# Optimization experiments

Hardware: AMD Instinct MI355X
Metric: run time of the kernel (lower is better)

Reference implementation:

```python
import jax, jax.numpy as jnp
import numpy as np

N_NODES = 50000
N_INC = 300000
IN_DIM = 256
OUT_DIM = 256
NEG_SLOPE = 0.2
BN_EPS = 1e-5


def setup_inputs() -> dict:
    key = jax.random.key(0)
    ks = jax.random.split(key, 8)
    x = jax.random.normal(ks[0], (N_NODES, IN_DIM), dtype=jnp.float32)
    node_idx = jax.random.randint(ks[1], (N_INC,), 0, N_NODES)
    edge_idx = jax.random.randint(ks[2], (N_INC,), 0, 20000)
    W = jax.random.normal(ks[3], (IN_DIM, OUT_DIM), dtype=jnp.float32) / np.sqrt(IN_DIM)
    att = jax.random.normal(ks[4], (2 * OUT_DIM,), dtype=jnp.float32) * 0.1
    bias = jnp.zeros((OUT_DIM,), dtype=jnp.float32)
    gamma = jnp.ones((OUT_DIM,), dtype=jnp.float32)
    beta = jnp.zeros((OUT_DIM,), dtype=jnp.float32)
    return {
        'x': x, 'node_idx': node_idx, 'edge_idx': edge_idx,
        'num_hyperedges': 20000,
        'W': W, 'att': att, 'bias': bias, 'gamma': gamma, 'beta': beta,
    }


def reference(x, node_idx, edge_idx, num_hyperedges, W, att, bias, gamma, beta):
    N = x.shape[0]
    M = num_hyperedges
    xw = x @ W                                  # [N, D]

    # attention over incidences (old-PyG: edge feature := node feature at edge id)
    x_i = xw[node_idx]                          # [E, D]
    x_j = xw[edge_idx]                          # [E, D]
    alpha = jnp.sum(jnp.concatenate([x_i, x_j], axis=-1) * att, axis=-1)  # [E]
    alpha = jax.nn.leaky_relu(alpha, NEG_SLOPE)
    # segment softmax grouped by node index
    amax = jax.ops.segment_max(alpha, node_idx, num_segments=N)
    amax = jnp.where(jnp.isfinite(amax), amax, 0.0)
    e = jnp.exp(alpha - amax[node_idx])
    esum = jax.ops.segment_sum(e, node_idx, num_segments=N)
    alpha = e / (esum[node_idx] + 1e-16)        # [E]

    ones = jnp.ones_like(alpha)
    Dn = jax.ops.segment_sum(ones, node_idx, num_segments=N)   # node degree
    Dinv = jnp.where(Dn > 0, 1.0 / Dn, 0.0)
    Be = jax.ops.segment_sum(ones, edge_idx, num_segments=M)   # edge degree
    Binv = jnp.where(Be > 0, 1.0 / Be, 0.0)

    # stage 1: node -> hyperedge, norm = B at target edge
    msg1 = (Binv[edge_idx] * alpha)[:, None] * x_i              # [E, D]
    edge_feat = jax.ops.segment_sum(msg1, edge_idx, num_segments=M)  # [M, D]

    # stage 2: hyperedge -> node, norm = D at target node
    msg2 = (Dinv[node_idx] * alpha)[:, None] * edge_feat[edge_idx]   # [E, D]
    out = jax.ops.segment_sum(msg2, node_idx, num_segments=N) + bias  # [N, D]

    # BatchNorm1d (training: batch stats, biased variance) + ELU
    mu = jnp.mean(out, axis=0)
    var = jnp.mean((out - mu) ** 2, axis=0)
    out = gamma * (out - mu) * jax.lax.rsqrt(var + BN_EPS) + beta
    return jax.nn.elu(out)
```

## Files before the change

kernel.cpp:

```cpp
#include <hip/hip_runtime.h>

#define N_NODES 50000
#define N_INC   300000
#define DIM     256
#define M_EDGES 20000
#define NEG_SLOPE 0.2f
#define BN_EPS  1e-5f
#define EBLK 20
#define NBLK 49

typedef __attribute__((ext_vector_type(8))) short short8;
typedef __attribute__((ext_vector_type(4))) float f32x4;

__device__ __forceinline__ unsigned bf16rn(float f) {
    unsigned u = __float_as_uint(f);
    return (u + 0x7FFFu + ((u >> 16) & 1u)) >> 16;
}
__device__ __forceinline__ float4 unp4(uint2 p) {
    return make_float4(__uint_as_float(p.x << 16),
                       __uint_as_float(p.x & 0xFFFF0000u),
                       __uint_as_float(p.y << 16),
                       __uint_as_float(p.y & 0xFFFF0000u));
}

__global__ void wt_kernel(const float* __restrict__ W, ushort* __restrict__ WT)
{
    int i = blockIdx.x * 256 + threadIdx.x;
    int k = i >> 8, n = i & 255;
    WT[n * 256 + k] = (ushort)bf16rn(W[i]);
}

#define GBM 256
__global__ __launch_bounds__(512) void gemm_persist(
    const float* __restrict__ A, const ushort* __restrict__ WT,
    const float* __restrict__ att,
    ushort* __restrict__ xwb, float* __restrict__ s1, float* __restrict__ s2)
{
    __shared__ __align__(16) char Bs[131072];
    int tid = threadIdx.x;
    int lane = tid & 63, w = tid >> 6;

    #pragma unroll
    for (int i = 0; i < 16; ++i) {
        int flat = tid + 512 * i;
        int n = flat >> 5, kc = flat & 31;
        uint4 v = *(const uint4*)(WT + n * 256 + kc * 8);
        int off = n * 512 + ((kc * 16) ^ ((n & 7) << 4));
        *(uint4*)(Bs + off) = v;
    }
    __syncthreads();

    int row0 = blockIdx.x * GBM + w * 32;

    short8 afrag[2][8];
    #pragma unroll
    for (int j = 0; j < 8; ++j) {
        #pragma unroll
        for (int s = 0; s < 2; ++s) {
            int row = row0 + s * 16 + (lane & 15);
            float4 u0 = make_float4(0.f, 0.f, 0.f, 0.f), u1 = u0;
            if (row < N_NODES) {
                const float* p = A + (size_t)row * DIM + j * 32 + (lane >> 4) * 8;
                u0 = *(const float4*)p;
                u1 = *(const float4*)(p + 4);
            }
            uint4 q;
            q.x = bf16rn(u0.x) | (bf16rn(u0.y) << 16);
            q.y = bf16rn(u0.z) | (bf16rn(u0.w) << 16);
            q.z = bf16rn(u1.x) | (bf16rn(u1.y) << 16);
            q.w = bf16rn(u1.z) | (bf16rn(u1.w) << 16);
            afrag[s][j] = *(short8*)&q;
        }
    }

    float p1a[2][4] = {}, p2a[2][4] = {};
    #pragma unroll
    for (int ch = 0; ch < 2; ++ch) {
        f32x4 acc[2][8] = {};
        #pragma unroll
        for (int j = 0; j < 8; ++j) {
            int kb = j * 64 + (lane >> 4) * 16;
            #pragma unroll
            for (int c = 0; c < 8; ++c) {
                int col = ch * 128 + c * 16 + (lane & 15);
                short8 b = *(const short8*)(Bs + col * 512 + (kb ^ ((col & 7) << 4)));
                acc[0][c] = __builtin_amdgcn_mfma_f32_16x16x32_bf16(afrag[0][j], b, acc[0][c], 0, 0, 0);
                acc[1][c] = __builtin_amdgcn_mfma_f32_16x16x32_bf16(afrag[1][j], b, acc[1][c], 0, 0, 0);
            }
        }
        #pragma unroll
        for (int c = 0; c < 8; ++c) {
            int col = ch * 128 + c * 16 + (lane & 15);
            float a1 = att[col], a2 = att[DIM + col];
            #pragma unroll
            for (int s = 0; s < 2; ++s)
                #pragma unroll
                for (int r = 0; r < 4; ++r) {
                    int row = row0 + s * 16 + (lane >> 4) * 4 + r;
                    float v = acc[s][c][r];
                    if (row < N_NODES)
                        xwb[(size_t)row * DIM + col] = (ushort)bf16rn(v);
                    p1a[s][r] += v * a1;
                    p2a[s][r] += v * a2;
                }
        }
    }
    #pragma unroll
    for (int s = 0; s < 2; ++s)
        #pragma unroll
        for (int r = 0; r < 4; ++r) {
            float p1 = p1a[s][r], p2 = p2a[s][r];
            #pragma unroll
            for (int msk = 1; msk < 16; msk <<= 1) {
                p1 += __shfl_xor(p1, msk);
                p2 += __shfl_xor(p2, msk);
            }
            int row = row0 + s * 16 + (lane >> 4) * 4 + r;
            if ((lane & 15) == 0 && row < N_NODES) {
                s1[row] = p1;
                s2[row] = p2;
            }
        }
}

__global__ void rank_kernel(
    const int* __restrict__ node_idx, const int* __restrict__ edge_idx,
    const float* __restrict__ s1, const float* __restrict__ s2,
    float* __restrict__ ealpha, unsigned* __restrict__ rank_pk,
    int* __restrict__ cnt_n, int* __restrict__ cnt_e)
{
    int e = blockIdx.x * blockDim.x + threadIdx.x;
    if (e >= N_INC) return;
    int n = node_idx[e], h = edge_idx[e];
    float a = s1[n] + s2[h];
    a = a > 0.f ? a : NEG_SLOPE * a;
    ealpha[e] = __expf(a);
    unsigned rn = (unsigned)atomicAdd(cnt_n + n, 1);
    unsigned re = (unsigned)atomicAdd(cnt_e + h, 1);
    rank_pk[e] = (re << 16) | rn;
}

__global__ __launch_bounds__(1024) void scan_partial(
    const int* __restrict__ cnt_e, int* __restrict__ start_e, int* __restrict__ totals_e,
    const int* __restrict__ cnt_n, int* __restrict__ start_n, int* __restrict__ totals_n)
{
    int b = blockIdx.x;
    const int* cnt; int* start; int* totals; int n; int cb;
    if (b < EBLK) { cnt = cnt_e; start = start_e; totals = totals_e; n = M_EDGES; cb = b; }
    else          { cnt = cnt_n; start = start_n; totals = totals_n; n = N_NODES; cb = b - EBLK; }
    int tid = threadIdx.x, lane = tid & 63, wid = tid >> 6;
    int i = cb * 1024 + tid;
    int v = (i < n) ? cnt[i] : 0;
    #pragma unroll
    for (int off = 1; off < 64; off <<= 1) {
        int t = __shfl_up(v, off);
        if (lane >= off) v += t;
    }
    __shared__ int wsum[16];
    if (lane == 63) wsum[wid] = v;
    __syncthreads();
    if (wid == 0 && lane < 16) {
        int s = wsum[lane];
        #pragma unroll
        for (int off = 1; off < 16; off <<= 1) {
            int t = __shfl_up(s, off);
            if (lane >= off) s += t;
        }
        wsum[lane] = s;
    }
    __syncthreads();
    if (wid > 0) v += wsum[wid - 1];
    if (i < n) start[i + 1] = v;
    if (tid == 1023) totals[cb] = v;
}

__global__ void scan_totals(
    const int* __restrict__ totals_e, int* __restrict__ boff_e,
    const int* __restrict__ totals_n, int* __restrict__ boff_n,
    int* __restrict__ start_e, int* __restrict__ start_n)
{
    int lane = threadIdx.x;
    int ve0 = (lane < EBLK) ? totals_e[lane] : 0;
    int ve = ve0;
    #pragma unroll
    for (int off = 1; off < 64; off <<= 1) {
        int t = __shfl_up(ve, off);
        if (lane >= off) ve += t;
    }
    if (lane < EBLK) boff_e[lane] = ve - ve0;
    int vn0 = (lane < NBLK) ? totals_n[lane] : 0;
    int vn = vn0;
    #pragma unroll
    for (int off = 1; off < 64; off <<= 1) {
        int t = __shfl_up(vn, off);
        if (lane >= off) vn += t;
    }
    if (lane < NBLK) boff_n[lane] = vn - vn0;
    if (lane == 0) { start_e[0] = 0; start_n[0] = 0; }
}

__global__ void scan_add(
    int* __restrict__ start_e, const int* __restrict__ boff_e,
    int* __restrict__ start_n, const int* __restrict__ boff_n)
{
    int id = blockIdx.x * 256 + threadIdx.x;
    if (id < M_EDGES) start_e[id + 1] += boff_e[id >> 10];
    else if (id < M_EDGES + N_NODES) {
        int j = id - M_EDGES;
        start_n[j + 1] += boff_n[j >> 10];
    }
}

__global__ void place_kernel(
    const int* __restrict__ node_idx, const int* __restrict__ edge_idx,
    const unsigned* __restrict__ rank_pk,
    const int* __restrict__ start_e, const int* __restrict__ start_n,
    int* __restrict__ list_e, int* __restrict__ list_n)
{
    int e = blockIdx.x * blockDim.x + threadIdx.x;
    if (e >= N_INC) return;
    unsigned pk = rank_pk[e];
    list_e[start_e[edge_idx[e]] + (pk >> 16)] = e;
    list_n[start_n[node_idx[e]] + (pk & 0xFFFFu)] = e;
}

__global__ void rnorm_kernel(
    const float* __restrict__ ealpha, const int* __restrict__ start_n,
    const int* __restrict__ list_n, float* __restrict__ rnorm)
{
    int n = blockIdx.x * blockDim.x + threadIdx.x;
    if (n >= N_NODES) return;
    int j0 = start_n[n], j1 = start_n[n + 1];
    float s = 0.f;
    for (int j = j0; j < j1; ++j) s += ealpha[list_n[j]];
    rnorm[n] = 1.f / (s + 1e-16f);
}

__global__ __launch_bounds__(256) void stage1_kernel(
    const ushort* __restrict__ xwb, const int* __restrict__ node_idx,
    const float* __restrict__ ealpha, const float* __restrict__ rnorm,
    const int* __restrict__ start_e, const int* __restrict__ list_e,
    ushort* __restrict__ edge_feat)
{
    int h = blockIdx.x * 4 + (threadIdx.x >> 6);
    if (h >= M_EDGES) return;
    int lane = threadIdx.x & 63;
    int j0 = start_e[h], j1 = start_e[h + 1];
    float4 acc = make_float4(0.f, 0.f, 0.f, 0.f);
    float4 ac2 = make_float4(0.f, 0.f, 0.f, 0.f);
    for (int base = j0; base < j1; base += 64) {
        int cnt = min(64, j1 - base);
        float wv = 0.f; int nv = 0;
        if (lane < cnt) {
            int e = list_e[base + lane];
            int n_ = node_idx[e];
            wv = ealpha[e] * rnorm[n_];
            nv = n_;
        }
        int jj = 0;
        for (; jj + 4 <= cnt; jj += 4) {
            float wg0 = __shfl(wv, jj);     int n0 = __shfl(nv, jj);
            float wg1 = __shfl(wv, jj + 1); int n1 = __shfl(nv, jj + 1);
            float wg2 = __shfl(wv, jj + 2); int n2 = __shfl(nv, jj + 2);
            float wg3 = __shfl(wv, jj + 3); int n3 = __shfl(nv, jj + 3);
            uint2 p0 = *(const uint2*)(xwb + (size_t)n0 * DIM + lane * 4);
            uint2 p1 = *(const uint2*)(xwb + (size_t)n1 * DIM + lane * 4);
            uint2 p2 = *(const uint2*)(xwb + (size_t)n2 * DIM + lane * 4);
            uint2 p3 = *(const uint2*)(xwb + (size_t)n3 * DIM + lane * 4);
            float4 v0 = unp4(p0), v1 = unp4(p1), v2 = unp4(p2), v3 = unp4(p3);
            acc.x += wg0 * v0.x + wg1 * v1.x;  ac2.x += wg2 * v2.x + wg3 * v3.x;
            acc.y += wg0 * v0.y + wg1 * v1.y;  ac2.y += wg2 * v2.y + wg3 * v3.y;
            acc.z += wg0 * v0.z + wg1 * v1.z;  ac2.z += wg2 * v2.z + wg3 * v3.z;
            acc.w += wg0 * v0.w + wg1 * v1.w;  ac2.w += wg2 * v2.w + wg3 * v3.w;
        }
        for (; jj < cnt; ++jj) {
            float wg = __shfl(wv, jj); int n0 = __shfl(nv, jj);
            float4 v = unp4(*(const uint2*)(xwb + (size_t)n0 * DIM + lane * 4));
            acc.x += wg * v.x; acc.y += wg * v.y;
            acc.z += wg * v.z; acc.w += wg * v.w;
        }
    }
    acc.x += ac2.x; acc.y += ac2.y; acc.z += ac2.z; acc.w += ac2.w;
    float binv = (j1 > j0) ? 1.f / (float)(j1 - j0) : 0.f;
    uint2 p;
    p.x = bf16rn(acc.x * binv) | (bf16rn(acc.y * binv) << 16);
    p.y = bf16rn(acc.z * binv) | (bf16rn(acc.w * binv) << 16);
    *(uint2*)(edge_feat + (size_t)h * DIM + lane * 4) = p;
}

__global__ __launch_bounds__(256) void stage2_kernel(
    const ushort* __restrict__ edge_feat, const int* __restrict__ edge_idx,
    const float* __restrict__ ealpha, const float* __restrict__ rnorm,
    const int* __restrict__ start_n, const int* __restrict__ list_n,
    const float* __restrict__ bias, float* __restrict__ out)
{
    int n = blockIdx.x * 4 + (threadIdx.x >> 6);
    if (n >= N_NODES) return;
    int lane = threadIdx.x & 63;
    int j0 = start_n[n], j1 = start_n[n + 1];
    float4 acc = make_float4(0.f, 0.f, 0.f, 0.f);
    float4 ac2 = make_float4(0.f, 0.f, 0.f, 0.f);
    for (int base = j0; base < j1; base += 64) {
        int cnt = min(64, j1 - base);
        float wv = 0.f; int hv = 0;
        if (lane < cnt) { int e = list_n[base + lane]; wv = ealpha[e]; hv = edge_idx[e]; }
        int jj = 0;
        for (; jj + 4 <= cnt; jj += 4) {
            float wg0 = __shfl(wv, jj);     int h0 = __shfl(hv, jj);
            float wg1 = __shfl(wv, jj + 1); int h1 = __shfl(hv, jj + 1);
            float wg2 = __shfl(wv, jj + 2); int h2 = __shfl(hv, jj + 2);
            float wg3 = __shfl(wv, jj + 3); int h3 = __shfl(hv, jj + 3);
            uint2 p0 = *(const uint2*)(edge_feat + (size_t)h0 * DIM + lane * 4);
            uint2 p1 = *(const uint2*)(edge_feat + (size_t)h1 * DIM + lane * 4);
            uint2 p2 = *(const uint2*)(edge_feat + (size_t)h2 * DIM + lane * 4);
            uint2 p3 = *(const uint2*)(edge_feat + (size_t)h3 * DIM + lane * 4);
            float4 v0 = unp4(p0), v1 = unp4(p1), v2 = unp4(p2), v3 = unp4(p3);
            acc.x += wg0 * v0.x + wg1 * v1.x;  ac2.x += wg2 * v2.x + wg3 * v3.x;
            acc.y += wg0 * v0.y + wg1 * v1.y;  ac2.y += wg2 * v2.y + wg3 * v3.y;
            acc.z += wg0 * v0.z + wg1 * v1.z;  ac2.z += wg2 * v2.z + wg3 * v3.z;
            acc.w += wg0 * v0.w + wg1 * v1.w;  ac2.w += wg2 * v2.w + wg3 * v3.w;
        }
        for (; jj < cnt; ++jj) {
            float wg = __shfl(wv, jj); int h0 = __shfl(hv, jj);
            float4 v = unp4(*(const uint2*)(edge_feat + (size_t)h0 * DIM + lane * 4));
            acc.x += wg * v.x; acc.y += wg * v.y;
            acc.z += wg * v.z; acc.w += wg * v.w;
        }
    }
    acc.x += ac2.x; acc.y += ac2.y; acc.z += ac2.z; acc.w += ac2.w;
    float sc = (j1 > j0) ? rnorm[n] / (float)(j1 - j0) : 0.f;
    float4 b = *(const float4*)(bias + lane * 4);
    acc.x = fmaf(acc.x, sc, b.x); acc.y = fmaf(acc.y, sc, b.y);
    acc.z = fmaf(acc.z, sc, b.z); acc.w = fmaf(acc.w, sc, b.w);
    *(float4*)(out + (size_t)n * DIM + lane * 4) = acc;
}

__global__ __launch_bounds__(256) void stats_kernel(
    const float* __restrict__ out, float* __restrict__ stats)
{
    __shared__ float lsum[4][256], lsq[4][256];
    int tid = threadIdx.x, lane = tid & 63, w = tid >> 6;
    int c4 = lane * 4;
    int rows_per = (N_NODES + gridDim.x - 1) / gridDim.x;
    int r0 = blockIdx.x * rows_per;
    int r1 = min(r0 + rows_per, N_NODES);
    float4 s = make_float4(0.f, 0.f, 0.f, 0.f);
    float4 q = make_float4(0.f, 0.f, 0.f, 0.f);
    for (int r = r0 + w; r < r1; r += 4) {
        float4 v = *(const float4*)(out + (size_t)r * DIM + c4);
        s.x += v.x; s.y += v.y; s.z += v.z; s.w += v.w;
        q.x += v.x * v.x; q.y += v.y * v.y; q.z += v.z * v.z; q.w += v.w * v.w;
    }
    *(float4*)&lsum[w][c4] = s;
    *(float4*)&lsq[w][c4] = q;
    __syncthreads();
    if (w == 0) {
        #pragma unroll
        for (int i = 1; i < 4; ++i) {
            s.x += lsum[i][c4]; s.y += lsum[i][c4 + 1]; s.z += lsum[i][c4 + 2]; s.w += lsum[i][c4 + 3];
            q.x += lsq[i][c4];  q.y += lsq[i][c4 + 1];  q.z += lsq[i][c4 + 2];  q.w += lsq[i][c4 + 3];
        }
        atomicAdd(stats + c4 + 0, s.x); atomicAdd(stats + c4 + 1, s.y);
        atomicAdd(stats + c4 + 2, s.z); atomicAdd(stats + c4 + 3, s.w);
        atomicAdd(stats + DIM + c4 + 0, q.x); atomicAdd(stats + DIM + c4 + 1, q.y);
        atomicAdd(stats + DIM + c4 + 2, q.z); atomicAdd(stats + DIM + c4 + 3, q.w);
    }
}

__global__ void bnprep_kernel(
    const float* __restrict__ stats, const float* __restrict__ gamma,
    const float* __restrict__ beta, float* __restrict__ scale, float* __restrict__ shift)
{
    int c = threadIdx.x;
    float mu = stats[c] * (1.f / N_NODES);
    float var = stats[DIM + c] * (1.f / N_NODES) - mu * mu;
    float sc = gamma[c] * rsqrtf(var + BN_EPS);
    scale[c] = sc;
    shift[c] = beta[c] - mu * sc;
}

__global__ __launch_bounds__(256) void bn_kernel(
    float* __restrict__ out, const float* __restrict__ scale, const float* __restrict__ shift)
{
    int idx = blockIdx.x * 256 + threadIdx.x;
    int c4 = (idx & 63) * 4;
    float4 sc = *(const float4*)(scale + c4);
    float4 sh = *(const float4*)(shift + c4);
    float4 v = ((float4*)out)[idx];
    v.x = fmaf(v.x, sc.x, sh.x); v.y = fmaf(v.y, sc.y, sh.y);
    v.z = fmaf(v.z, sc.z, sh.z); v.w = fmaf(v.w, sc.w, sh.w);
    v.x = v.x > 0.f ? v.x : __expf(v.x) - 1.f;
    v.y = v.y > 0.f ? v.y : __expf(v.y) - 1.f;
    v.z = v.z > 0.f ? v.z : __expf(v.z) - 1.f;
    v.w = v.w > 0.f ? v.w : __expf(v.w) - 1.f;
    ((float4*)out)[idx] = v;
}

extern "C" void kernel_launch(void* const* d_in, const int* in_sizes, int n_in,
                              void* d_out, int out_size, void* d_ws, size_t ws_size,
                              hipStream_t stream)
{
    const float* x        = (const float*)d_in[0];
    const int*   node_idx = (const int*)d_in[1];
    const int*   edge_idx = (const int*)d_in[2];
    const float* W        = (const float*)d_in[4];
    const float* att      = (const float*)d_in[5];
    const float* bias     = (const float*)d_in[6];
    const float* gamma    = (const float*)d_in[7];
    const float* beta     = (const float*)d_in[8];
    float* out = (float*)d_out;
    ushort* xwb = (ushort*)d_out;

    ushort* edge_feat = (ushort*)d_ws;
    int*   cnt_e   = (int*)(edge_feat + (size_t)M_EDGES * DIM);
    int*   cnt_n   = cnt_e + M_EDGES;
    float* stats   = (float*)(cnt_n + N_NODES);
    float* s1      = stats + 2 * DIM;
    float* s2      = s1 + N_NODES;
    float* ealpha  = s2 + N_NODES;
    unsigned* rank_pk = (unsigned*)(ealpha + N_INC);
    float* rnorm   = (float*)(rank_pk + N_INC);
    int*   start_e = (int*)(rnorm + N_NODES);
    int*   start_n = start_e + M_EDGES + 1;
    int*   list_e  = start_n + N_NODES + 1;
    int*   list_n  = list_e + N_INC;
    ushort* WT     = (ushort*)(list_n + N_INC);
    int*   totals_e = (int*)(WT + 256 * 256);
    int*   boff_e   = totals_e + EBLK;
    int*   totals_n = boff_e + EBLK;
    int*   boff_n   = totals_n + NBLK;
    float* scale    = (float*)(boff_n + NBLK);
    float* shift    = scale + DIM;

    hipMemsetAsync(cnt_e, 0, (size_t)(M_EDGES + N_NODES + 2 * DIM) * 4, stream);

    wt_kernel<<<256, 256, 0, stream>>>(W, WT);
    gemm_persist<<<(N_NODES + GBM - 1) / GBM, 512, 0, stream>>>(x, WT, att, xwb, s1, s2);
    rank_kernel<<<(N_INC + 255) / 256, 256, 0, stream>>>(node_idx, edge_idx, s1, s2, ealpha, rank_pk, cnt_n, cnt_e);
    scan_partial<<<EBLK + NBLK, 1024, 0, stream>>>(cnt_e, start_e, totals_e, cnt_n, start_n, totals_n);
    scan_totals<<<1, 64, 0, stream>>>(totals_e, boff_e, totals_n, boff_n, start_e, start_n);
    scan_add<<<(M_EDGES + N_NODES + 255) / 256, 256, 0, stream>>>(start_e, boff_e, start_n, boff_n);
    place_kernel<<<(N_INC + 255) / 256, 256, 0, stream>>>(node_idx, edge_idx, rank_pk, start_e, start_n, list_e, list_n);
    rnorm_kernel<<<(N_NODES + 255) / 256, 256, 0, stream>>>(ealpha, start_n, list_n, rnorm);
    stage1_kernel<<<(M_EDGES + 3) / 4, 256, 0, stream>>>(xwb, node_idx, ealpha, rnorm, start_e, list_e, edge_feat);
    stage2_kernel<<<(N_NODES + 3) / 4, 256, 0, stream>>>(edge_feat, edge_idx, ealpha, rnorm, start_n, list_n, bias, out);
    stats_kernel<<<128, 256, 0, stream>>>(out, stats);
    bnprep_kernel<<<1, 256, 0, stream>>>(stats, gamma, beta, scale, shift);
    bn_kernel<<<N_NODES * DIM / 4 / 256, 256, 0, stream>>>(out, scale, shift);
}
```

Before: 207.4 us.

## Stage GEMM output through LDS for coalesced stores and fuse scan kernels

The GEMM now computes all 256 output columns in a single pass. It stages the bf16 results in shared memory per wave and then writes them to xwb as coalesced 16-byte rows, replacing the scattered 2-byte stores. The scan_totals kernel is folded into scan_add, which removes one launch and the boff buffers. The rank kernel handles two incidences per thread, the stats grid is enlarged, and launch_bounds adds a minimum of two blocks per CU. Holding twice as many accumulator registers may spill or lower occupancy, and with 128KB of LDS per block the two-blocks hint may not be achievable.

```diff
diff --git a/kernel.cpp b/kernel.cpp
--- a/kernel.cpp
+++ b/kernel.cpp
@@ -2,6 +2,7 @@
 
 #define N_NODES 50000
 #define N_INC   300000
+#define RHALF   150000
 #define DIM     256
 #define M_EDGES 20000
 #define NEG_SLOPE 0.2f
@@ -31,7 +32,7 @@
 }
 
 #define GBM 256
-__global__ __launch_bounds__(512) void gemm_persist(
+__global__ __launch_bounds__(512, 2) void gemm_persist(
     const float* __restrict__ A, const ushort* __restrict__ WT,
     const float* __restrict__ att,
     ushort* __restrict__ xwb, float* __restrict__ s1, float* __restrict__ s2)
@@ -73,37 +74,31 @@
         }
     }
 
+    f32x4 acc[2][16] = {};
+    #pragma unroll
+    for (int j = 0; j < 8; ++j) {
+        int kb = j * 64 + (lane >> 4) * 16;
+        #pragma unroll
+        for (int c = 0; c < 16; ++c) {
+            int col = c * 16 + (lane & 15);
+            short8 b = *(const short8*)(Bs + col * 512 + (kb ^ ((col & 7) << 4)));
+            acc[0][c] = __builtin_amdgcn_mfma_f32_16x16x32_bf16(afrag[0][j], b, acc[0][c], 0, 0, 0);
+            acc[1][c] = __builtin_amdgcn_mfma_f32_16x16x32_bf16(afrag[1][j], b, acc[1][c], 0, 0, 0);
+        }
+    }
+
     float p1a[2][4] = {}, p2a[2][4] = {};
     #pragma unroll
-    for (int ch = 0; ch < 2; ++ch) {
-        f32x4 acc[2][8] = {};
-        #pragma unroll
-        for (int j = 0; j < 8; ++j) {
-            int kb = j * 64 + (lane >> 4) * 16;
+    for (int c = 0; c < 16; ++c) {
+        int col = c * 16 + (lane & 15);
+        float a1 = att[col], a2 = att[DIM + col];
+        #pragma unroll
+        for (int s = 0; s < 2; ++s)
             #pragma unroll
-            for (int c = 0; c < 8; ++c) {
-                int col = ch * 128 + c * 16 + (lane & 15);
-                short8 b = *(const short8*)(Bs + col * 512 + (kb ^ ((col & 7) << 4)));
-                acc[0][c] = __builtin_amdgcn_mfma_f32_16x16x32_bf16(afrag[0][j], b, acc[0][c], 0, 0, 0);
-                acc[1][c] = __builtin_amdgcn_mfma_f32_16x16x32_bf16(afrag[1][j], b, acc[1][c], 0, 0, 0);
+            for (int r = 0; r < 4; ++r) {
+                p1a[s][r] += acc[s][c][r] * a1;
+                p2a[s][r] += acc[s][c][r] * a2;
             }
-        }
-        #pragma unroll
-        for (int c = 0; c < 8; ++c) {
-            int col = ch * 128 + c * 16 + (lane & 15);
-            float a1 = att[col], a2 = att[DIM + col];
-            #pragma unroll
-            for (int s = 0; s < 2; ++s)
-                #pragma unroll
-                for (int r = 0; r < 4; ++r) {
-                    int row = row0 + s * 16 + (lane >> 4) * 4 + r;
-                    float v = acc[s][c][r];
-                    if (row < N_NODES)
-                        xwb[(size_t)row * DIM + col] = (ushort)bf16rn(v);
-                    p1a[s][r] += v * a1;
-                    p2a[s][r] += v * a2;
-                }
-        }
     }
     #pragma unroll
     for (int s = 0; s < 2; ++s)
@@ -121,6 +116,31 @@
                 s2[row] = p2;
             }
         }
+
+    __syncthreads();
+    char* slice = Bs + w * 16384;
+    #pragma unroll
+    for (int c = 0; c < 16; ++c) {
+        #pragma unroll
+        for (int s = 0; s < 2; ++s)
+            #pragma unroll
+            for (int r = 0; r < 4; ++r) {
+                int lrow = s * 16 + (lane >> 4) * 4 + r;
+                int col = c * 16 + (lane & 15);
+                *(ushort*)(slice + lrow * 512 + col * 2) = (ushort)bf16rn(acc[s][c][r]);
+            }
+    }
+    __syncthreads();
+    #pragma unroll
+    for (int i = 0; i < 16; ++i) {
+        int flat = lane + 64 * i;
+        int lrow = flat >> 5, c16 = flat & 31;
+        int row = row0 + lrow;
+        if (row < N_NODES) {
+            uint4 v = *(const uint4*)(slice + lrow * 512 + c16 * 16);
+            *(uint4*)(xwb + (size_t)row * DIM + c16 * 8) = v;
+        }
+    }
 }
 
 __global__ void rank_kernel(
@@ -130,14 +150,22 @@
     int* __restrict__ cnt_n, int* __restrict__ cnt_e)
 {
     int e = blockIdx.x * blockDim.x + threadIdx.x;
-    if (e >= N_INC) return;
-    int n = node_idx[e], h = edge_idx[e];
-    float a = s1[n] + s2[h];
-    a = a > 0.f ? a : NEG_SLOPE * a;
-    ealpha[e] = __expf(a);
-    unsigned rn = (unsigned)atomicAdd(cnt_n + n, 1);
-    unsigned re = (unsigned)atomicAdd(cnt_e + h, 1);
-    rank_pk[e] = (re << 16) | rn;
+    if (e >= RHALF) return;
+    int e2 = e + RHALF;
+    int n0 = node_idx[e],  h0 = edge_idx[e];
+    int n1 = node_idx[e2], h1 = edge_idx[e2];
+    float a0 = s1[n0] + s2[h0];
+    float a1 = s1[n1] + s2[h1];
+    a0 = a0 > 0.f ? a0 : NEG_SLOPE * a0;
+    a1 = a1 > 0.f ? a1 : NEG_SLOPE * a1;
+    ealpha[e]  = __expf(a0);
+    ealpha[e2] = __expf(a1);
+    unsigned rn0 = (unsigned)atomicAdd(cnt_n + n0, 1);
+    unsigned re0 = (unsigned)atomicAdd(cnt_e + h0, 1);
+    unsigned rn1 = (unsigned)atomicAdd(cnt_n + n1, 1);
+    unsigned re1 = (unsigned)atomicAdd(cnt_e + h1, 1);
+    rank_pk[e]  = (re0 << 16) | rn0;
+    rank_pk[e2] = (re1 << 16) | rn1;
 }
 
 __global__ __launch_bounds__(1024) void scan_partial(
@@ -174,40 +202,39 @@
     if (tid == 1023) totals[cb] = v;
 }
 
-__global__ void scan_totals(
-    const int* __restrict__ totals_e, int* __restrict__ boff_e,
-    const int* __restrict__ totals_n, int* __restrict__ boff_n,
-    int* __restrict__ start_e, int* __restrict__ start_n)
-{
-    int lane = threadIdx.x;
-    int ve0 = (lane < EBLK) ? totals_e[lane] : 0;
-    int ve = ve0;
-    #pragma unroll
-    for (int off = 1; off < 64; off <<= 1) {
-        int t = __shfl_up(ve, off);
-        if (lane >= off) ve += t;
-    }
-    if (lane < EBLK) boff_e[lane] = ve - ve0;
-    int vn0 = (lane < NBLK) ? totals_n[lane] : 0;
-    int vn = vn0;
-    #pragma unroll
-    for (int off = 1; off < 64; off <<= 1) {
-        int t = __shfl_up(vn, off);
-        if (lane >= off) vn += t;
-    }
-    if (lane < NBLK) boff_n[lane] = vn - vn0;
-    if (lane == 0) { start_e[0] = 0; start_n[0] = 0; }
-}
-
-__global__ void scan_add(
-    int* __restrict__ start_e, const int* __restrict__ boff_e,
-    int* __restrict__ start_n, const int* __restrict__ boff_n)
-{
-    int id = blockIdx.x * 256 + threadIdx.x;
-    if (id < M_EDGES) start_e[id + 1] += boff_e[id >> 10];
+__global__ __launch_bounds__(256) void scan_add(
+    int* __restrict__ start_e, const int* __restrict__ totals_e,
+    int* __restrict__ start_n, const int* __restrict__ totals_n)
+{
+    __shared__ int lboff_e[EBLK], lboff_n[NBLK];
+    int tid = threadIdx.x;
+    if (tid < 64) {
+        int lane = tid;
+        int ve0 = (lane < EBLK) ? totals_e[lane] : 0;
+        int ve = ve0;
+        #pragma unroll
+        for (int off = 1; off < 64; off <<= 1) {
+            int t = __shfl_up(ve, off);
+            if (lane >= off) ve += t;
+        }
+        if (lane < EBLK) lboff_e[lane] = ve - ve0;
+        int vn0 = (lane < NBLK) ? totals_n[lane] : 0;
+        int vn = vn0;
+        #pragma unroll
+        for (int off = 1; off < 64; off <<= 1) {
+            int t = __shfl_up(vn, off);
+            if (lane >= off) vn += t;
+        }
+        if (lane < NBLK) lboff_n[lane] = vn - vn0;
+    }
+    __syncthreads();
+    int id = blockIdx.x * 256 + tid;
+    if (id == 0) start_e[0] = 0;
+    if (id < M_EDGES) start_e[id + 1] += lboff_e[id >> 10];
     else if (id < M_EDGES + N_NODES) {
         int j = id - M_EDGES;
-        start_n[j + 1] += boff_n[j >> 10];
+        if (j == 0) start_n[0] = 0;
+        start_n[j + 1] += lboff_n[j >> 10];
     }
 }
 
@@ -426,25 +453,22 @@
     int*   list_n  = list_e + N_INC;
     ushort* WT     = (ushort*)(list_n + N_INC);
     int*   totals_e = (int*)(WT + 256 * 256);
-    int*   boff_e   = totals_e + EBLK;
-    int*   totals_n = boff_e + EBLK;
-    int*   boff_n   = totals_n + NBLK;
-    float* scale    = (float*)(boff_n + NBLK);
+    int*   totals_n = totals_e + EBLK;
+    float* scale    = (float*)(totals_n + NBLK);
     float* shift    = scale + DIM;
 
     hipMemsetAsync(cnt_e, 0, (size_t)(M_EDGES + N_NODES + 2 * DIM) * 4, stream);
 
     wt_kernel<<<256, 256, 0, stream>>>(W, WT);
     gemm_persist<<<(N_NODES + GBM - 1) / GBM, 512, 0, stream>>>(x, WT, att, xwb, s1, s2);
-    rank_kernel<<<(N_INC + 255) / 256, 256, 0, stream>>>(node_idx, edge_idx, s1, s2, ealpha, rank_pk, cnt_n, cnt_e);
+    rank_kernel<<<(RHALF + 255) / 256, 256, 0, stream>>>(node_idx, edge_idx, s1, s2, ealpha, rank_pk, cnt_n, cnt_e);
     scan_partial<<<EBLK + NBLK, 1024, 0, stream>>>(cnt_e, start_e, totals_e, cnt_n, start_n, totals_n);
-    scan_totals<<<1, 64, 0, stream>>>(totals_e, boff_e, totals_n, boff_n, start_e, start_n);
-    scan_add<<<(M_EDGES + N_NODES + 255) / 256, 256, 0, stream>>>(start_e, boff_e, start_n, boff_n);
+    scan_add<<<(M_EDGES + N_NODES + 255) / 256, 256, 0, stream>>>(start_e, totals_e, start_n, totals_n);
     place_kernel<<<(N_INC + 255) / 256, 256, 0, stream>>>(node_idx, edge_idx, rank_pk, start_e, start_n, list_e, list_n);
     rnorm_kernel<<<(N_NODES + 255) / 256, 256, 0, stream>>>(ealpha, start_n, list_n, rnorm);
     stage1_kernel<<<(M_EDGES + 3) / 4, 256, 0, stream>>>(xwb, node_idx, ealpha, rnorm, start_e, list_e, edge_feat);
     stage2_kernel<<<(N_NODES + 3) / 4, 256, 0, stream>>>(edge_feat, edge_idx, ealpha, rnorm, start_n, list_n, bias, out);
-    stats_kernel<<<128, 256, 0, stream>>>(out, stats);
+    stats_kernel<<<200, 256, 0, stream>>>(out, stats);
     bnprep_kernel<<<1, 256, 0, stream>>>(stats, gamma, beta, scale, shift);
     bn_kernel<<<N_NODES * DIM / 4 / 256, 256, 0, stream>>>(out, scale, shift);
 }
```

New measurement: 207.4 us. No clear change (-0.0%).
